# Performance work log

Hardware: AMD Instinct MI355X
Metric: run time of the kernel (lower is better)

The kernel has to match this reference:

```python
import jax, jax.numpy as jnp
import numpy as np

B, C, H, W = 4, 256, 128, 256
NUM_CODES = 256  # codebook rows; dim_code == C


def setup_inputs() -> dict:
    key = jax.random.key(0)
    k_feat, k_code = jax.random.split(key)
    feature = jax.random.normal(k_feat, (B, C, H, W), dtype=jnp.float32)
    codebook = jax.random.normal(k_code, (NUM_CODES, C), dtype=jnp.float32)
    return {"feature": feature, "codebook": codebook}


def reference(feature, codebook):
    # Faithful to ComminPub.sender core:
    #   weights = (feature_expand * codebooks).sum(dim=2) / (codebooks*codebooks).sum(dim=2)
    # expressed as a contraction over C instead of materializing [B,N,C,H,W].
    code_norm = jnp.sum(codebook * codebook, axis=1)          # [N]
    weights = jnp.einsum('bchw,nc->bnhw', feature, codebook)   # [B,N,H,W]
    weights = weights / code_norm[None, :, None, None]
    # fc_after_rbdc reconstruction: einsum('b n h w, n c -> b c h w', weights, codebook)
    recon = jnp.einsum('bnhw,nc->bchw', weights, codebook)     # [B,C,H,W]
    return recon
```

## Files before the change

kernel.cpp:

```cpp
#include <hip/hip_runtime.h>
#include <hip/hip_bf16.h>
#include <cstdint>

#define CDIM   256
#define NCODES 256
#define HWB    32768
#define BATCH  4
#define BN     64
#define BK     32

typedef __bf16 bf16x8 __attribute__((ext_vector_type(8)));
typedef float  f32x4  __attribute__((ext_vector_type(4)));

__global__ __launch_bounds__(256) void prep_kernel(const float* __restrict__ cb,
                                                   __bf16* __restrict__ Mb) {
    __shared__ float s[NCODES];
    const int i = blockIdx.x;
    const int j = threadIdx.x;

    const float* row = cb + (size_t)j * CDIM;
    float nrm = 0.f;
#pragma unroll 8
    for (int c = 0; c < CDIM; c += 4) {
        f32x4 v = *(const f32x4*)(row + c);
        nrm += v[0] * v[0] + v[1] * v[1] + v[2] * v[2] + v[3] * v[3];
    }
    s[j] = cb[(size_t)j * CDIM + i] / nrm;
    __syncthreads();

    float acc = 0.f;
#pragma unroll 16
    for (int n = 0; n < NCODES; ++n)
        acc += s[n] * cb[(size_t)n * CDIM + j];
    Mb[(size_t)i * CDIM + j] = (__bf16)acc;
}

__global__ __launch_bounds__(256, 4) void recon_kernel(
    const float* __restrict__ feat, const __bf16* __restrict__ Mb,
    float* __restrict__ out) {
    __shared__ __align__(16) __bf16 Alds[2][CDIM * BK];
    __shared__ __align__(16) __bf16 Blds[2][BN * BK];

    const int tid  = threadIdx.x;
    const int lane = tid & 63;
    const int w    = tid >> 6;
    const int quad = lane >> 4;
    const int l16  = lane & 15;

    const int b  = blockIdx.y;
    const int p0 = blockIdx.x * BN;

    const float* fbase = feat + ((size_t)b * CDIM) * HWB + p0;
    float*       obase = out  + ((size_t)b * CDIM) * HWB + p0;

    f32x4 acc[4][4];
#pragma unroll
    for (int mt = 0; mt < 4; ++mt)
#pragma unroll
        for (int nt = 0; nt < 4; ++nt)
            acc[mt][nt] = (f32x4){0.f, 0.f, 0.f, 0.f};

    const float* fp0 = fbase + (size_t)(w * 8) * HWB + lane;
    const int bw_off = lane * BK + (w ^ (lane & 3)) * 8;
    const int qsrcA = (lane & 3) ^ ((lane >> 2) & 3);
    const int qrd = (quad ^ (l16 & 3)) * 8;

    {
        float fv[8];
#pragma unroll
        for (int j = 0; j < 8; ++j) fv[j] = fp0[(size_t)j * HWB];
#pragma unroll
        for (int j = 0; j < 4; ++j) {
            const int gbase = j * 256 + (w << 6);
            const int r = (gbase + lane) >> 2;
            const __bf16* gsrc = Mb + (size_t)r * CDIM + qsrcA * 8;
            __builtin_amdgcn_global_load_lds(
                (const __attribute__((address_space(1))) void*)gsrc,
                (__attribute__((address_space(3))) void*)(&Alds[0][0] + (size_t)gbase * 8),
                16, 0, 0);
        }
        bf16x8 pk;
#pragma unroll
        for (int j = 0; j < 8; ++j) pk[j] = (__bf16)fv[j];
        *(bf16x8*)(&Blds[0][0] + bw_off) = pk;
    }
    __syncthreads();

    int cur = 0;
    for (int kc = 0; kc < 8; ++kc) {
        const bool pf = (kc + 1 < 8);
        float fv[8];
        if (pf) {
            const float* fp = fp0 + (size_t)(kc + 1) * BK * HWB;
#pragma unroll
            for (int j = 0; j < 8; ++j) fv[j] = fp[(size_t)j * HWB];
#pragma unroll
            for (int j = 0; j < 4; ++j) {
                const int gbase = j * 256 + (w << 6);
                const int r = (gbase + lane) >> 2;
                const __bf16* gsrc = Mb + (size_t)r * CDIM + (kc + 1) * BK + qsrcA * 8;
                __builtin_amdgcn_global_load_lds(
                    (const __attribute__((address_space(1))) void*)gsrc,
                    (__attribute__((address_space(3))) void*)(&Alds[cur ^ 1][0] + (size_t)gbase * 8),
                    16, 0, 0);
            }
        }

        bf16x8 bfr[4];
#pragma unroll
        for (int nt = 0; nt < 4; ++nt)
            bfr[nt] = *(const bf16x8*)(&Blds[cur][0] + (nt * 16 + l16) * BK + qrd);
#pragma unroll
        for (int mt = 0; mt < 4; ++mt) {
            bf16x8 af = *(const bf16x8*)(&Alds[cur][0] + (w * 64 + mt * 16 + l16) * BK + qrd);
#pragma unroll
            for (int nt = 0; nt < 4; ++nt)
                acc[mt][nt] = __builtin_amdgcn_mfma_f32_16x16x32_bf16(
                    af, bfr[nt], acc[mt][nt], 0, 0, 0);
        }

        if (pf) {
            bf16x8 pk;
#pragma unroll
            for (int j = 0; j < 8; ++j) pk[j] = (__bf16)fv[j];
            *(bf16x8*)(&Blds[cur ^ 1][0] + bw_off) = pk;
        }
        __syncthreads();
        cur ^= 1;
    }

#pragma unroll
    for (int mt = 0; mt < 4; ++mt) {
#pragma unroll
        for (int r = 0; r < 4; ++r) {
            const int c = w * 64 + mt * 16 + quad * 4 + r;
            float* orow = obase + (size_t)c * HWB + l16;
#pragma unroll
            for (int nt = 0; nt < 4; ++nt)
                orow[nt * 16] = acc[mt][nt][r];
        }
    }
}

extern "C" void kernel_launch(void* const* d_in, const int* in_sizes, int n_in,
                              void* d_out, int out_size, void* d_ws, size_t ws_size,
                              hipStream_t stream) {
    const float* feat = (const float*)d_in[0];
    const float* cb   = (const float*)d_in[1];
    float* out = (float*)d_out;

    __bf16* Mb = (__bf16*)d_ws;

    prep_kernel<<<NCODES, 256, 0, stream>>>(cb, Mb);

    dim3 grid(HWB / BN, BATCH);
    recon_kernel<<<grid, 256, 0, stream>>>(feat, Mb, out);
}
```

Baseline: 253.5 us.

## Keep projection matrix in registers and run persistent blocks over pixel tiles

The recon kernel now loads its 32-row slice of the bf16 projection matrix into registers once per block and reuses it across four 128-pixel tiles. It launches 256 persistent blocks of 512 threads instead of a 2D grid. This removes the per-k-chunk LDS staging of the matrix and cuts repeated loads of Mb. Feature loads are prefetched three chunks ahead into registers, with a hand-written waitcnt/barrier around a double-buffered LDS tile. The cost is much higher register pressure and fewer, larger blocks, which may reduce occupancy and memory-latency hiding for this bandwidth-bound kernel.

```diff
diff --git a/kernel.cpp b/kernel.cpp
--- a/kernel.cpp
+++ b/kernel.cpp
@@ -6,8 +6,9 @@
 #define NCODES 256
 #define HWB    32768
 #define BATCH  4
-#define BN     64
-#define BK     32
+#define BN     128
+#define NTILES 4
+#define TPB    512
 
 typedef __bf16 bf16x8 __attribute__((ext_vector_type(8)));
 typedef float  f32x4  __attribute__((ext_vector_type(4)));
@@ -35,110 +36,88 @@
     Mb[(size_t)i * CDIM + j] = (__bf16)acc;
 }
 
-__global__ __launch_bounds__(256, 4) void recon_kernel(
+__global__ __launch_bounds__(TPB, 2) void recon_kernel(
     const float* __restrict__ feat, const __bf16* __restrict__ Mb,
     float* __restrict__ out) {
-    __shared__ __align__(16) __bf16 Alds[2][CDIM * BK];
-    __shared__ __align__(16) __bf16 Blds[2][BN * BK];
+    __shared__ __align__(16) __bf16 Blds[2][BN * 32];
 
     const int tid  = threadIdx.x;
     const int lane = tid & 63;
     const int w    = tid >> 6;
     const int quad = lane >> 4;
     const int l16  = lane & 15;
+    const int r0   = w * 32;
 
-    const int b  = blockIdx.y;
-    const int p0 = blockIdx.x * BN;
+    const __bf16* mb = Mb + (size_t)(r0 + l16) * CDIM + quad * 8;
+    bf16x8 mreg[2][8];
+#pragma unroll
+    for (int mt = 0; mt < 2; ++mt)
+#pragma unroll
+        for (int kc = 0; kc < 8; ++kc)
+            mreg[mt][kc] = *(const bf16x8*)(mb + (size_t)mt * 16 * CDIM + kc * 32);
 
-    const float* fbase = feat + ((size_t)b * CDIM) * HWB + p0;
-    float*       obase = out  + ((size_t)b * CDIM) * HWB + p0;
+    const int spx   = lane + (w & 1) * 64;
+    const int sk0   = (w >> 1) * 8;
+    const int swoff = spx * 32 + (((w >> 1) ^ ((spx >> 1) & 3)) * 8);
+    const int rdoff = (quad ^ ((l16 >> 1) & 3)) * 8;
 
-    f32x4 acc[4][4];
+    const int b        = blockIdx.x >> 6;
+    const int px_base0 = (blockIdx.x & 63) * (BN * NTILES);
+
+    const float* fB = feat + (size_t)b * CDIM * HWB;
+    float*       oB = out  + (size_t)b * CDIM * HWB;
+
+    for (int ti = 0; ti < NTILES; ++ti) {
+        const int p0 = px_base0 + ti * BN;
+        const float* fs = fB + p0 + spx + (size_t)sk0 * HWB;
+
+        float fv[3][8];
 #pragma unroll
-    for (int mt = 0; mt < 4; ++mt)
+        for (int c = 0; c < 3; ++c)
 #pragma unroll
-        for (int nt = 0; nt < 4; ++nt)
-            acc[mt][nt] = (f32x4){0.f, 0.f, 0.f, 0.f};
+            for (int j = 0; j < 8; ++j)
+                fv[c][j] = fs[(size_t)(c * 32 + j) * HWB];
 
-    const float* fp0 = fbase + (size_t)(w * 8) * HWB + lane;
-    const int bw_off = lane * BK + (w ^ (lane & 3)) * 8;
-    const int qsrcA = (lane & 3) ^ ((lane >> 2) & 3);
-    const int qrd = (quad ^ (l16 & 3)) * 8;
+        f32x4 acc[2][8];
+#pragma unroll
+        for (int mt = 0; mt < 2; ++mt)
+#pragma unroll
+            for (int nt = 0; nt < 8; ++nt)
+                acc[mt][nt] = (f32x4){0.f, 0.f, 0.f, 0.f};
 
-    {
-        float fv[8];
 #pragma unroll
-        for (int j = 0; j < 8; ++j) fv[j] = fp0[(size_t)j * HWB];
+        for (int i = 0; i < 8; ++i) {
+            bf16x8 pk;
 #pragma unroll
-        for (int j = 0; j < 4; ++j) {
-            const int gbase = j * 256 + (w << 6);
-            const int r = (gbase + lane) >> 2;
-            const __bf16* gsrc = Mb + (size_t)r * CDIM + qsrcA * 8;
-            __builtin_amdgcn_global_load_lds(
-                (const __attribute__((address_space(1))) void*)gsrc,
-                (__attribute__((address_space(3))) void*)(&Alds[0][0] + (size_t)gbase * 8),
-                16, 0, 0);
-        }
-        bf16x8 pk;
+            for (int j = 0; j < 8; ++j) pk[j] = (__bf16)fv[i % 3][j];
+            if (i < 5) {
 #pragma unroll
-        for (int j = 0; j < 8; ++j) pk[j] = (__bf16)fv[j];
-        *(bf16x8*)(&Blds[0][0] + bw_off) = pk;
-    }
-    __syncthreads();
-
-    int cur = 0;
-    for (int kc = 0; kc < 8; ++kc) {
-        const bool pf = (kc + 1 < 8);
-        float fv[8];
-        if (pf) {
-            const float* fp = fp0 + (size_t)(kc + 1) * BK * HWB;
+                for (int j = 0; j < 8; ++j)
+                    fv[i % 3][j] = fs[(size_t)((i + 3) * 32 + j) * HWB];
+            }
+            *(bf16x8*)(&Blds[i & 1][0] + swoff) = pk;
+            asm volatile("s_waitcnt lgkmcnt(0)\n\ts_barrier" ::: "memory");
 #pragma unroll
-            for (int j = 0; j < 8; ++j) fv[j] = fp[(size_t)j * HWB];
-#pragma unroll
-            for (int j = 0; j < 4; ++j) {
-                const int gbase = j * 256 + (w << 6);
-                const int r = (gbase + lane) >> 2;
-                const __bf16* gsrc = Mb + (size_t)r * CDIM + (kc + 1) * BK + qsrcA * 8;
-                __builtin_amdgcn_global_load_lds(
-                    (const __attribute__((address_space(1))) void*)gsrc,
-                    (__attribute__((address_space(3))) void*)(&Alds[cur ^ 1][0] + (size_t)gbase * 8),
-                    16, 0, 0);
+            for (int nt = 0; nt < 8; ++nt) {
+                bf16x8 bfr = *(const bf16x8*)(
+                    &Blds[i & 1][0] + (nt * 16 + l16) * 32 + rdoff);
+                acc[0][nt] = __builtin_amdgcn_mfma_f32_16x16x32_bf16(
+                    mreg[0][i], bfr, acc[0][nt], 0, 0, 0);
+                acc[1][nt] = __builtin_amdgcn_mfma_f32_16x16x32_bf16(
+                    mreg[1][i], bfr, acc[1][nt], 0, 0, 0);
             }
         }
 
-        bf16x8 bfr[4];
+        float* ob = oB + p0 + l16;
 #pragma unroll
-        for (int nt = 0; nt < 4; ++nt)
-            bfr[nt] = *(const bf16x8*)(&Blds[cur][0] + (nt * 16 + l16) * BK + qrd);
+        for (int mt = 0; mt < 2; ++mt)
 #pragma unroll
-        for (int mt = 0; mt < 4; ++mt) {
-            bf16x8 af = *(const bf16x8*)(&Alds[cur][0] + (w * 64 + mt * 16 + l16) * BK + qrd);
+            for (int r = 0; r < 4; ++r) {
+                float* orow = ob + (size_t)(r0 + mt * 16 + quad * 4 + r) * HWB;
 #pragma unroll
-            for (int nt = 0; nt < 4; ++nt)
-                acc[mt][nt] = __builtin_amdgcn_mfma_f32_16x16x32_bf16(
-                    af, bfr[nt], acc[mt][nt], 0, 0, 0);
-        }
-
-        if (pf) {
-            bf16x8 pk;
-#pragma unroll
-            for (int j = 0; j < 8; ++j) pk[j] = (__bf16)fv[j];
-            *(bf16x8*)(&Blds[cur ^ 1][0] + bw_off) = pk;
-        }
-        __syncthreads();
-        cur ^= 1;
-    }
-
-#pragma unroll
-    for (int mt = 0; mt < 4; ++mt) {
-#pragma unroll
-        for (int r = 0; r < 4; ++r) {
-            const int c = w * 64 + mt * 16 + quad * 4 + r;
-            float* orow = obase + (size_t)c * HWB + l16;
-#pragma unroll
-            for (int nt = 0; nt < 4; ++nt)
-                orow[nt * 16] = acc[mt][nt][r];
-        }
+                for (int nt = 0; nt < 8; ++nt)
+                    orow[nt * 16] = acc[mt][nt][r];
+            }
     }
 }
 
@@ -153,6 +132,5 @@
 
     prep_kernel<<<NCODES, 256, 0, stream>>>(cb, Mb);
 
-    dim3 grid(HWB / BN, BATCH);
-    recon_kernel<<<grid, 256, 0, stream>>>(feat, Mb, out);
+    recon_kernel<<<256, TPB, 0, stream>>>(feat, Mb, out);
 }
```

Result: no change. 257.8 us (+1.7%).
